# Kernel tuning notes

Hardware: AMD Instinct MI355X
Metric: run time of the kernel (lower is better)

Reference implementation:

```python
import jax, jax.numpy as jnp
import numpy as np

D_MODEL = 1024
K_QUERY = 32
K_TOPK = 4

def setup_inputs() -> dict:
    key = jax.random.key(0)
    k1, k2, k3, k4, k5 = jax.random.split(key, 5)
    x = jax.random.normal(k1, (4, 2048, D_MODEL), dtype=jnp.float32)
    # nn.Linear(d_model, k_query): weight [k_query, d_model], bias [k_query]
    sc = 1.0 / np.sqrt(D_MODEL)
    Wq = jax.random.uniform(k2, (K_QUERY, D_MODEL), jnp.float32, -sc, sc)
    bq = jax.random.uniform(k3, (K_QUERY,), jnp.float32, -sc, sc)
    Wk = jax.random.uniform(k4, (K_QUERY, D_MODEL), jnp.float32, -sc, sc)
    bk = jax.random.uniform(k5, (K_QUERY,), jnp.float32, -sc, sc)
    return {"x": x, "Wq": Wq, "bq": bq, "Wk": Wk, "bk": bk}

def reference(x, Wq, bq, Wk, bk):
    # x: [B, T, D]
    queries = jnp.einsum('btd,kd->btk', x, Wq) + bq      # [B, T, Kq]
    keys = jnp.einsum('btd,kd->btk', x, Wk) + bk         # [B, T, Kq]
    sim = jnp.einsum('btk,bsk->bts', queries, keys)      # [B, T, T]
    sim = sim / jnp.sqrt(jnp.float32(queries.shape[-1]))
    _, topk_idx = jax.lax.top_k(sim, K_TOPK)              # [B, T, K]
    # gather neighbors per (b, t): x[b, topk_idx[b, t]] -> [B, T, K, D]
    neighbors = jax.vmap(lambda xb, ib: xb[ib])(x, topk_idx)
    gathered = neighbors.mean(axis=2)                     # [B, T, D]
    return gathered
```

## Files before the change

kernel.cpp:

```cpp
#include <hip/hip_runtime.h>
#include <math.h>

#define D_MODEL 1024
#define T_SEQ   2048
#define NBATCH  4
#define NROWS   (NBATCH * T_SEQ)
#define NOUT    64

#define SKLD 520
#define SQLD 20
#define XLD  1032

typedef double v4df __attribute__((ext_vector_type(4)));

__device__ __forceinline__ bool key_gt(float av, int ai, float bv, int bi) {
    return (av > bv) || (av == bv && ai < bi);
}

__device__ __forceinline__ void cmpswap(float& v0, int& i0, float& v1, int& i1) {
    bool sw = key_gt(v1, i1, v0, i0);
    float nv0 = sw ? v1 : v0, nv1 = sw ? v0 : v1;
    int   ni0 = sw ? i1 : i0, ni1 = sw ? i0 : i1;
    v0 = nv0; v1 = nv1; i0 = ni0; i1 = ni1;
}

__device__ __forceinline__ void merge4(float (&a)[4], int (&ai)[4],
                                       float b0, int j0, float b1, int j1,
                                       float b2, int j2, float b3, int j3) {
    if (!key_gt(a[0], ai[0], b3, j3)) { a[0] = b3; ai[0] = j3; }
    if (!key_gt(a[1], ai[1], b2, j2)) { a[1] = b2; ai[1] = j2; }
    if (!key_gt(a[2], ai[2], b1, j1)) { a[2] = b1; ai[2] = j1; }
    if (!key_gt(a[3], ai[3], b0, j0)) { a[3] = b0; ai[3] = j0; }
    cmpswap(a[0], ai[0], a[2], ai[2]);
    cmpswap(a[1], ai[1], a[3], ai[3]);
    cmpswap(a[0], ai[0], a[1], ai[1]);
    cmpswap(a[2], ai[2], a[3], ai[3]);
}

__device__ __forceinline__ void insert4(float (&tv)[4], int (&tix)[4], float v, int idx) {
    if (v > tv[3]) {
        bool g0 = v > tv[0], g1 = v > tv[1], g2 = v > tv[2];
        float n0 = g0 ? v : tv[0];
        int   m0 = g0 ? idx : tix[0];
        float n1 = g1 ? (g0 ? tv[0] : v) : tv[1];
        int   m1 = g1 ? (g0 ? tix[0] : idx) : tix[1];
        float n2 = g2 ? (g1 ? tv[1] : v) : tv[2];
        int   m2 = g2 ? (g1 ? tix[1] : idx) : tix[2];
        float n3 = g2 ? tv[2] : v;
        int   m3 = g2 ? tix[2] : idx;
        tv[0] = n0; tv[1] = n1; tv[2] = n2; tv[3] = n3;
        tix[0] = m0; tix[1] = m1; tix[2] = m2; tix[3] = m3;
    }
}

__device__ void run_probe(int tid, int* __restrict__ tab)
{
    __shared__ double Aref[16][4];
    __shared__ double Bref[4][16];
    __shared__ double Dref[16][16];

    const int lane = tid;
    if (tid < 64) {
        const int m = lane & 15, k = lane >> 4;
        Aref[m][k] = (double)(1 + m * 4 + k);
        Bref[k][m] = (double)(1 + k * 16 + m);
    }
    __syncthreads();
    {
        const int e = tid;
        const int m = e >> 4, n = e & 15;
        double s = 0.0;
        for (int k = 0; k < 4; ++k) s += Aref[m][k] * Bref[k][n];
        Dref[m][n] = s;
    }
    __syncthreads();

    if (tid >= 64) return;

    int found = -1;
    for (int h = 0; h < 16; ++h) {
        if (found >= 0) break;
        const int fa = h & 1, fb = (h >> 1) & 1, fd = h >> 2;
        const int am = fa ? (lane >> 2) : (lane & 15);
        const int ak = fa ? (lane & 3)  : (lane >> 4);
        const int bn = fb ? (lane >> 2) : (lane & 15);
        const int bk = fb ? (lane & 3)  : (lane >> 4);
        v4df c = {0.0, 0.0, 0.0, 0.0};
        c = __builtin_amdgcn_mfma_f64_16x16x4f64(Aref[am][ak], Bref[bk][bn], c, 0, 0, 0);
        bool ok = true;
        #pragma unroll
        for (int i = 0; i < 4; ++i) {
            int dm, dn;
            if (fd == 0)      { dm = 4 * (lane >> 4) + i; dn = lane & 15; }
            else if (fd == 1) { dn = 4 * (lane >> 4) + i; dm = lane & 15; }
            else if (fd == 2) { dm = (lane >> 4) + 4 * i; dn = lane & 15; }
            else              { dn = (lane >> 4) + 4 * i; dm = lane & 15; }
            if (c[i] != Dref[dm][dn]) ok = false;
        }
        if (__all(ok)) found = h;
    }

    const int fa = (found >= 0) ? (found & 1) : 0;
    const int fb = (found >= 0) ? ((found >> 1) & 1) : 0;
    const int fd = (found >= 0) ? (found >> 2) : 0;
    tab[1   + lane] = fa ? (lane >> 2) : (lane & 15);
    tab[65  + lane] = fa ? (lane & 3)  : (lane >> 4);
    tab[129 + lane] = fb ? (lane & 3)  : (lane >> 4);
    tab[193 + lane] = fb ? (lane >> 2) : (lane & 15);
    #pragma unroll
    for (int i = 0; i < 4; ++i) {
        int dm, dn;
        if (fd == 0)      { dm = 4 * (lane >> 4) + i; dn = lane & 15; }
        else if (fd == 1) { dn = 4 * (lane >> 4) + i; dm = lane & 15; }
        else if (fd == 2) { dm = (lane >> 4) + 4 * i; dn = lane & 15; }
        else              { dn = (lane >> 4) + 4 * i; dm = lane & 15; }
        tab[257 + lane * 4 + i] = dm;
        tab[513 + lane * 4 + i] = dn;
    }
    if (lane == 0) tab[0] = found;
}

__global__ __launch_bounds__(256) void wprep_probe(
    const float* __restrict__ Wq, const float* __restrict__ Wk,
    double* __restrict__ Wdt, int* __restrict__ tab)
{
    const int tid = threadIdx.x;
    const int idx = blockIdx.x * 256 + tid;
    const int o = idx & 63;
    const int d = idx >> 6;
    float v = (o < 32) ? Wq[(size_t)o * D_MODEL + d]
                       : Wk[(size_t)(o - 32) * D_MODEL + d];
    Wdt[(size_t)d * 64 + o] = (double)v;

    if (blockIdx.x == 0) run_probe(tid, tab);
}

__global__ __launch_bounds__(512) void proj_mfma(
    const float* __restrict__ x, const double* __restrict__ Wdt,
    const float* __restrict__ bq, const float* __restrict__ bk_,
    const int* __restrict__ tab,
    float* __restrict__ Qt, float* __restrict__ Kt)
{
    __shared__ float  xlds[16 * XLD];
    __shared__ double comb[4][64][4];

    const int tid  = threadIdx.x;
    const int lane = tid & 63;
    const int wav  = tid >> 6;
    const int og   = __builtin_amdgcn_readfirstlane(wav >> 1);
    const int half = __builtin_amdgcn_readfirstlane(wav & 1);
    const int row0 = blockIdx.x * 16;
    const int dbase = half * 512;

    const int flag = tab[0];
    const int am  = tab[1   + lane];
    const int ak  = tab[65  + lane];
    const int bkk = tab[129 + lane];
    const int bn  = tab[193 + lane];

    const double* wcol = Wdt + og * 16;

    #pragma unroll
    for (int j = 0; j < 8; ++j) {
        const int f  = j * 512 + tid;
        const int r  = f >> 8;
        const int c4 = f & 255;
        float4 v = *reinterpret_cast<const float4*>(
            x + (size_t)(row0 + r) * D_MODEL + c4 * 4);
        *reinterpret_cast<float4*>(&xlds[r * XLD + c4 * 4]) = v;
    }
    __syncthreads();

    v4df acc = {0.0, 0.0, 0.0, 0.0};

    if (flag >= 0) {
        #pragma unroll 8
        for (int kk = 0; kk < 128; ++kk) {
            double a = (double)xlds[am * XLD + dbase + kk * 4 + ak];
            double b = wcol[(size_t)(dbase + kk * 4 + bkk) * 64 + bn];
            acc = __builtin_amdgcn_mfma_f64_16x16x4f64(a, b, acc, 0, 0, 0);
        }
    } else {
        const int n  = lane & 15;
        const int r4 = (lane >> 4) * 4;
        for (int dd = 0; dd < 512; ++dd) {
            const int d = dbase + dd;
            double wv = wcol[(size_t)d * 64 + n];
            #pragma unroll
            for (int i = 0; i < 4; ++i)
                acc[i] = fma((double)xlds[(r4 + i) * XLD + d], wv, acc[i]);
        }
    }

    if (half == 1) {
        #pragma unroll
        for (int i = 0; i < 4; ++i) comb[og][lane][i] = acc[i];
    }
    __syncthreads();

    if (half == 0) {
        #pragma unroll
        for (int i = 0; i < 4; ++i) {
            const double tot = acc[i] + comb[og][lane][i];
            const int dmv = tab[257 + lane * 4 + i];
            const int dnv = tab[513 + lane * 4 + i];
            const int out = og * 16 + dnv;
            const int row = row0 + dmv;
            const int bb  = row >> 11, t = row & 2047;
            const double bias = (out < 32) ? (double)bq[out] : (double)bk_[out - 32];
            const float v = (float)(tot + bias);
            if (out < 32) Qt[((size_t)bb * 32 + out) * T_SEQ + t] = v;
            else          Kt[((size_t)bb * 32 + (out - 32)) * T_SEQ + t] = v;
        }
    }
}

__global__ __launch_bounds__(256, 2) void sim_topk_gather(
    const float* __restrict__ x,
    const float* __restrict__ Qt, const float* __restrict__ Kt,
    float* __restrict__ out)
{
    __shared__ float klds[32 * SKLD];
    __shared__ float qlds[32 * SQLD];
    float (*cV)[16][4] = reinterpret_cast<float(*)[16][4]>(klds);
    int   (*cI)[16][4] = reinterpret_cast<int(*)[16][4]>(klds + 256);
    int   (*topIdx)[4] = reinterpret_cast<int(*)[4]>(klds + 512);

    const int tid  = threadIdx.x;
    const int lane = tid & 63;
    const int wav  = tid >> 6;
    const int tt   = blockIdx.x & 127;
    const int b    = blockIdx.x >> 7;
    const int tblk = tt * 16;

    const float* QtB = Qt + (size_t)b * 32 * T_SEQ;
    const float* KtB = Kt + (size_t)b * 32 * T_SEQ;

    if (tid < 128) {
        const int i  = tid >> 2;
        const int t4 = (tid & 3) * 4;
        float4 v = *reinterpret_cast<const float4*>(QtB + (size_t)i * T_SEQ + tblk + t4);
        *reinterpret_cast<float4*>(&qlds[i * SQLD + t4]) = v;
    }

    const int t0 = (tid & 3) * 4;
    const int s0 = (tid >> 2) * 8;

    float tv[4][4]; int tix[4][4];
    #pragma unroll
    for (int r = 0; r < 4; ++r)
        #pragma unroll
        for (int j = 0; j < 4; ++j) { tv[r][j] = -INFINITY; tix[r][j] = 0x7fffffff; }

    for (int st = 0; st < 4; ++st) {
        __syncthreads();
        #pragma unroll
        for (int j = 0; j < 16; ++j) {
            const int f  = tid + j * 256;
            const int ki = f >> 7;
            const int ks = (f & 127) * 4;
            float4 v = *reinterpret_cast<const float4*>(
                KtB + (size_t)ki * T_SEQ + st * 512 + ks);
            *reinterpret_cast<float4*>(&klds[ki * SKLD + ks]) = v;
        }
        __syncthreads();

        float acc[4][8];
        #pragma unroll
        for (int r = 0; r < 4; ++r)
            #pragma unroll
            for (int c = 0; c < 8; ++c) acc[r][c] = 0.f;

        #pragma unroll 4
        for (int i = 0; i < 32; ++i) {
            float4 qv  = *reinterpret_cast<const float4*>(&qlds[i * SQLD + t0]);
            float4 kv0 = *reinterpret_cast<const float4*>(&klds[i * SKLD + s0]);
            float4 kv1 = *reinterpret_cast<const float4*>(&klds[i * SKLD + s0 + 4]);
            const float qa[4] = {qv.x, qv.y, qv.z, qv.w};
            const float ka[8] = {kv0.x, kv0.y, kv0.z, kv0.w, kv1.x, kv1.y, kv1.z, kv1.w};
            #pragma unroll
            for (int r = 0; r < 4; ++r)
                #pragma unroll
                for (int c = 0; c < 8; ++c)
                    acc[r][c] = fmaf(qa[r], ka[c], acc[r][c]);
        }

        const int sbase = st * 512 + s0;
        #pragma unroll
        for (int c = 0; c < 8; ++c)
            #pragma unroll
            for (int r = 0; r < 4; ++r)
                insert4(tv[r], tix[r], acc[r][c], sbase + c);
    }

    #pragma unroll
    for (int m = 4; m <= 32; m <<= 1) {
        #pragma unroll
        for (int r = 0; r < 4; ++r) {
            float b0 = __shfl_xor(tv[r][0], m, 64);
            float b1 = __shfl_xor(tv[r][1], m, 64);
            float b2 = __shfl_xor(tv[r][2], m, 64);
            float b3 = __shfl_xor(tv[r][3], m, 64);
            int   j0 = __shfl_xor(tix[r][0], m, 64);
            int   j1 = __shfl_xor(tix[r][1], m, 64);
            int   j2 = __shfl_xor(tix[r][2], m, 64);
            int   j3 = __shfl_xor(tix[r][3], m, 64);
            merge4(tv[r], tix[r], b0, j0, b1, j1, b2, j2, b3, j3);
        }
    }

    __syncthreads();

    if (lane < 4) {
        #pragma unroll
        for (int r = 0; r < 4; ++r)
            #pragma unroll
            for (int j = 0; j < 4; ++j) {
                cV[wav][lane * 4 + r][j] = tv[r][j];
                cI[wav][lane * 4 + r][j] = tix[r][j];
            }
    }
    __syncthreads();

    if (tid < 16) {
        float mv[4]; int mi[4];
        #pragma unroll
        for (int j = 0; j < 4; ++j) { mv[j] = cV[0][tid][j]; mi[j] = cI[0][tid][j]; }
        #pragma unroll
        for (int w = 1; w < 4; ++w)
            merge4(mv, mi,
                   cV[w][tid][0], cI[w][tid][0],
                   cV[w][tid][1], cI[w][tid][1],
                   cV[w][tid][2], cI[w][tid][2],
                   cV[w][tid][3], cI[w][tid][3]);
        #pragma unroll
        for (int j = 0; j < 4; ++j) topIdx[tid][j] = mi[j];
    }
    __syncthreads();

    const float* xb = x + (size_t)b * T_SEQ * D_MODEL;
    float* ob = out + ((size_t)b * T_SEQ + tblk) * D_MODEL;
    #pragma unroll 4
    for (int r = 0; r < 16; ++r) {
        const int i0 = topIdx[r][0], i1 = topIdx[r][1], i2 = topIdx[r][2], i3 = topIdx[r][3];
        float4 a0 = *(reinterpret_cast<const float4*>(xb + (size_t)i0 * D_MODEL) + tid);
        float4 a1 = *(reinterpret_cast<const float4*>(xb + (size_t)i1 * D_MODEL) + tid);
        float4 a2 = *(reinterpret_cast<const float4*>(xb + (size_t)i2 * D_MODEL) + tid);
        float4 a3 = *(reinterpret_cast<const float4*>(xb + (size_t)i3 * D_MODEL) + tid);
        float4 o;
        o.x = (a0.x + a1.x + a2.x + a3.x) * 0.25f;
        o.y = (a0.y + a1.y + a2.y + a3.y) * 0.25f;
        o.z = (a0.z + a1.z + a2.z + a3.z) * 0.25f;
        o.w = (a0.w + a1.w + a2.w + a3.w) * 0.25f;
        *(reinterpret_cast<float4*>(ob + (size_t)r * D_MODEL) + tid) = o;
    }
}

extern "C" void kernel_launch(void* const* d_in, const int* in_sizes, int n_in,
                              void* d_out, int out_size, void* d_ws, size_t ws_size,
                              hipStream_t stream) {
    const float* x  = (const float*)d_in[0];
    const float* Wq = (const float*)d_in[1];
    const float* bq = (const float*)d_in[2];
    const float* Wk = (const float*)d_in[3];
    const float* bk = (const float*)d_in[4];
    float* out = (float*)d_out;

    char* wsb = (char*)d_ws;
    int*    tab  = (int*)wsb;
    double* Wdt  = (double*)(wsb + 4096);
    float*  Qt   = (float*)(wsb + 4096 + (size_t)D_MODEL * NOUT * 8);
    float*  Kt   = Qt + (size_t)NBATCH * 32 * T_SEQ;

    wprep_probe<<<dim3(256), dim3(256), 0, stream>>>(Wq, Wk, Wdt, tab);
    proj_mfma<<<dim3(NROWS / 16), dim3(512), 0, stream>>>(x, Wdt, bq, bk, tab, Qt, Kt);
    sim_topk_gather<<<dim3(512), dim3(256), 0, stream>>>(x, Qt, Kt, out);
}
```

Before: 162.3 us.

## Drop LDS staging in sim/topk kernel and halve query rows per block

The similarity/top-k kernel no longer stages K and Q tiles in shared memory; each thread reads Q and K directly from global memory (relying on L1/L2 caching). Each block now handles 8 query rows instead of 16, so twice as many blocks are launched, and each thread sweeps 2 chunks of 1024 keys. The launch-bounds occupancy hint rises from 2 to 4. This removes the LDS staging barriers and the shared-memory footprint in exchange for more redundant global/cache traffic for K, which is re-read by twice as many blocks.

```diff
diff --git a/kernel.cpp b/kernel.cpp
--- a/kernel.cpp
+++ b/kernel.cpp
@@ -7,9 +7,7 @@
 #define NROWS   (NBATCH * T_SEQ)
 #define NOUT    64
 
-#define SKLD 520
-#define SQLD 20
-#define XLD  1032
+#define XLD  1036
 
 typedef double v4df __attribute__((ext_vector_type(4)));
 
@@ -215,36 +213,27 @@
     }
 }
 
-__global__ __launch_bounds__(256, 2) void sim_topk_gather(
+__global__ __launch_bounds__(256, 4) void sim_topk_gather(
     const float* __restrict__ x,
     const float* __restrict__ Qt, const float* __restrict__ Kt,
     float* __restrict__ out)
 {
-    __shared__ float klds[32 * SKLD];
-    __shared__ float qlds[32 * SQLD];
-    float (*cV)[16][4] = reinterpret_cast<float(*)[16][4]>(klds);
-    int   (*cI)[16][4] = reinterpret_cast<int(*)[16][4]>(klds + 256);
-    int   (*topIdx)[4] = reinterpret_cast<int(*)[4]>(klds + 512);
+    __shared__ float cV[4][8][4];
+    __shared__ int   cI[4][8][4];
+    __shared__ int   topIdx[8][4];
 
     const int tid  = threadIdx.x;
     const int lane = tid & 63;
     const int wav  = tid >> 6;
-    const int tt   = blockIdx.x & 127;
-    const int b    = blockIdx.x >> 7;
-    const int tblk = tt * 16;
+    const int tt   = blockIdx.x & 255;
+    const int b    = blockIdx.x >> 8;
+    const int tblk = tt * 8;
+    const int tg   = tid & 1;
+    const int sg   = tid >> 1;
 
     const float* QtB = Qt + (size_t)b * 32 * T_SEQ;
     const float* KtB = Kt + (size_t)b * 32 * T_SEQ;
-
-    if (tid < 128) {
-        const int i  = tid >> 2;
-        const int t4 = (tid & 3) * 4;
-        float4 v = *reinterpret_cast<const float4*>(QtB + (size_t)i * T_SEQ + tblk + t4);
-        *reinterpret_cast<float4*>(&qlds[i * SQLD + t4]) = v;
-    }
-
-    const int t0 = (tid & 3) * 4;
-    const int s0 = (tid >> 2) * 8;
+    const int trow0 = tblk + tg * 4;
 
     float tv[4][4]; int tix[4][4];
     #pragma unroll
@@ -252,18 +241,9 @@
         #pragma unroll
         for (int j = 0; j < 4; ++j) { tv[r][j] = -INFINITY; tix[r][j] = 0x7fffffff; }
 
-    for (int st = 0; st < 4; ++st) {
-        __syncthreads();
-        #pragma unroll
-        for (int j = 0; j < 16; ++j) {
-            const int f  = tid + j * 256;
-            const int ki = f >> 7;
-            const int ks = (f & 127) * 4;
-            float4 v = *reinterpret_cast<const float4*>(
-                KtB + (size_t)ki * T_SEQ + st * 512 + ks);
-            *reinterpret_cast<float4*>(&klds[ki * SKLD + ks]) = v;
-        }
-        __syncthreads();
+    #pragma unroll
+    for (int sweep = 0; sweep < 2; ++sweep) {
+        const int s0 = sweep * 1024 + sg * 8;
 
         float acc[4][8];
         #pragma unroll
@@ -273,9 +253,9 @@
 
         #pragma unroll 4
         for (int i = 0; i < 32; ++i) {
-            float4 qv  = *reinterpret_cast<const float4*>(&qlds[i * SQLD + t0]);
-            float4 kv0 = *reinterpret_cast<const float4*>(&klds[i * SKLD + s0]);
-            float4 kv1 = *reinterpret_cast<const float4*>(&klds[i * SKLD + s0 + 4]);
+            float4 qv  = *reinterpret_cast<const float4*>(QtB + (size_t)i * T_SEQ + trow0);
+            float4 kv0 = *reinterpret_cast<const float4*>(KtB + (size_t)i * T_SEQ + s0);
+            float4 kv1 = *reinterpret_cast<const float4*>(KtB + (size_t)i * T_SEQ + s0 + 4);
             const float qa[4] = {qv.x, qv.y, qv.z, qv.w};
             const float ka[8] = {kv0.x, kv0.y, kv0.z, kv0.w, kv1.x, kv1.y, kv1.z, kv1.w};
             #pragma unroll
@@ -285,16 +265,15 @@
                     acc[r][c] = fmaf(qa[r], ka[c], acc[r][c]);
         }
 
-        const int sbase = st * 512 + s0;
         #pragma unroll
         for (int c = 0; c < 8; ++c)
             #pragma unroll
             for (int r = 0; r < 4; ++r)
-                insert4(tv[r], tix[r], acc[r][c], sbase + c);
-    }
-
-    #pragma unroll
-    for (int m = 4; m <= 32; m <<= 1) {
+                insert4(tv[r], tix[r], acc[r][c], s0 + c);
+    }
+
+    #pragma unroll
+    for (int m = 2; m <= 32; m <<= 1) {
         #pragma unroll
         for (int r = 0; r < 4; ++r) {
             float b0 = __shfl_xor(tv[r][0], m, 64);
@@ -309,9 +288,7 @@
         }
     }
 
-    __syncthreads();
-
-    if (lane < 4) {
+    if (lane < 2) {
         #pragma unroll
         for (int r = 0; r < 4; ++r)
             #pragma unroll
@@ -322,7 +299,7 @@
     }
     __syncthreads();
 
-    if (tid < 16) {
+    if (tid < 8) {
         float mv[4]; int mi[4];
         #pragma unroll
         for (int j = 0; j < 4; ++j) { mv[j] = cV[0][tid][j]; mi[j] = cI[0][tid][j]; }
@@ -341,7 +318,7 @@
     const float* xb = x + (size_t)b * T_SEQ * D_MODEL;
     float* ob = out + ((size_t)b * T_SEQ + tblk) * D_MODEL;
     #pragma unroll 4
-    for (int r = 0; r < 16; ++r) {
+    for (int r = 0; r < 8; ++r) {
         const int i0 = topIdx[r][0], i1 = topIdx[r][1], i2 = topIdx[r][2], i3 = topIdx[r][3];
         float4 a0 = *(reinterpret_cast<const float4*>(xb + (size_t)i0 * D_MODEL) + tid);
         float4 a1 = *(reinterpret_cast<const float4*>(xb + (size_t)i1 * D_MODEL) + tid);
@@ -374,5 +351,5 @@
 
     wprep_probe<<<dim3(256), dim3(256), 0, stream>>>(Wq, Wk, Wdt, tab);
     proj_mfma<<<dim3(NROWS / 16), dim3(512), 0, stream>>>(x, Wdt, bq, bk, tab, Qt, Kt);
-    sim_topk_gather<<<dim3(512), dim3(256), 0, stream>>>(x, Qt, Kt, out);
-}
+    sim_topk_gather<<<dim3(1024), dim3(256), 0, stream>>>(x, Qt, Kt, out);
+}
```

Result: no change. 160.0 us (-1.4%).
